# Performance work log

Measured on AMD Instinct MI355X. Metric: run time of the kernel, lower is better.

The kernel has to match this reference:

```python
import jax, jax.numpy as jnp
import numpy as np

# NCHW 3x3 conv, padding=1. BatchNorm (inference affine) is folded into conv weight/bias,
# which is mathematically identical to Conv->BN(eval) in the original.
def conv3(x, w, b, stride):
    y = jax.lax.conv_general_dilated(x, w, (stride, stride), [(1, 1), (1, 1)],
                                     dimension_numbers=('NCHW', 'OIHW', 'NCHW'))
    return y + b[None, :, None, None]

def lin1(x, w, b):  # 1x1 conv as channel matmul; w: [out, in]
    return jnp.einsum('oc,bchw->bohw', w, x) + b[None, :, None, None]

def setup_inputs():
    key = jax.random.key(0)
    ks = list(jax.random.split(key, 32))
    C, M = 32, 32  # cv_hypo_num, mid_dim (kq_dim == mid_dim since mid_dim <= 128)
    B, H, W = 1, 256, 512
    w3 = lambda k, o, i: jax.random.normal(k, (o, i, 3, 3), jnp.float32) * 0.05
    w1 = lambda k, o, i: jax.random.normal(k, (o, i), jnp.float32) * 0.05
    bv = lambda k, o: jax.random.normal(k, (o,), jnp.float32) * 0.01
    inp = {
        'mono_pseudo_cost': jax.random.normal(ks[0], (B, C, H, W), jnp.float32),
        'cost_volume': jax.random.normal(ks[1], (B, C, H, W), jnp.float32),
        # mono_expand / multi_expand: two stride-2 conv(+folded BN)+ReLU blocks each
        'me_w1': w3(ks[2], M, C), 'me_b1': bv(ks[3], M),
        'me_w2': w3(ks[4], M, C), 'me_b2': bv(ks[5], M),
        'xe_w1': w3(ks[6], M, C), 'xe_b1': bv(ks[7], M),
        'xe_w2': w3(ks[8], M, C), 'xe_b2': bv(ks[9], M),
        # 1x1 q/k/v projections for both branches
        'mq_w': w1(ks[10], M, M), 'mq_b': bv(ks[11], M),
        'mk_w': w1(ks[12], M, M), 'mk_b': bv(ks[13], M),
        'mv_w': w1(ks[14], M, M), 'mv_b': bv(ks[15], M),
        'xq_w': w1(ks[16], M, M), 'xq_b': bv(ks[17], M),
        'xk_w': w1(ks[18], M, M), 'xk_b': bv(ks[19], M),
        'xv_w': w1(ks[20], M, M), 'xv_b': bv(ks[21], M),
        # residual branches
        'mr_w1': w3(ks[22], M, C), 'mr_b1': bv(ks[23], M),
        'mr_w2': w3(ks[24], M, C), 'mr_b2': bv(ks[25], M),
        'xr_w': w1(ks[26], M, C), 'xr_b': bv(ks[27], M),
        'gamma': jnp.full((1,), 0.5, jnp.float32),  # nonzero so attention path is live
    }
    return inp

def reference(mono_pseudo_cost, cost_volume,
              me_w1, me_b1, me_w2, me_b2,
              xe_w1, xe_b1, xe_w2, xe_b2,
              mq_w, mq_b, mk_w, mk_b, mv_w, mv_b,
              xq_w, xq_b, xk_w, xk_b, xv_w, xv_b,
              mr_w1, mr_b1, mr_w2, mr_b2,
              xr_w, xr_b, gamma):
    relu = jax.nn.relu
    init_h, init_w = cost_volume.shape[2], cost_volume.shape[3]
    M = me_w1.shape[0]
    # feature extractors (stride-2 x2): [B,32,256,512] -> [B,32,64,128]
    mono_feat = relu(conv3(relu(conv3(mono_pseudo_cost, me_w1, me_b1, 2)), me_w2, me_b2, 2))
    multi_feat = relu(conv3(relu(conv3(cost_volume, xe_w1, xe_b1, 2)), xe_w2, xe_b2, 2))
    b, c, h, w = multi_feat.shape
    hw = h * w
    # q/k/v as [B, C, hw]
    mono_q = lin1(mono_feat, mq_w, mq_b).reshape(b, -1, hw)
    mono_k = lin1(mono_feat, mk_w, mk_b).reshape(b, -1, hw)
    mono_v = lin1(mono_feat, mv_w, mv_b).reshape(b, -1, hw)
    multi_q = lin1(multi_feat, xq_w, xq_b).reshape(b, -1, hw)
    multi_k = lin1(multi_feat, xk_w, xk_b).reshape(b, -1, hw)
    multi_v = lin1(multi_feat, xv_w, xv_b).reshape(b, -1, hw)
    # full [B, hw, hw] attention, no 1/sqrt(d) scaling (as in original)
    mono_atten = jax.nn.softmax(jnp.einsum('bci,bcj->bij', mono_q, mono_k), axis=-1)
    multi_atten = jax.nn.softmax(jnp.einsum('bci,bcj->bij', multi_q, multi_k), axis=-1)
    # cross application: mono values weighted by multi attention and vice versa
    mono_out = jnp.einsum('bcj,bij->bci', mono_v, multi_atten).reshape(b, M, h, w)
    multi_out = jnp.einsum('bcj,bij->bci', multi_v, mono_atten).reshape(b, M, h, w)
    fused = jnp.concatenate([multi_out, mono_out], axis=1)
    # nearest-neighbor upsample back to input size (integer factor 4)
    fused = jnp.repeat(jnp.repeat(fused, init_h // h, axis=2), init_w // w, axis=3)
    # residual branches
    mono_residual = relu(conv3(relu(conv3(mono_pseudo_cost, mr_w1, mr_b1, 1)), mr_w2, mr_b2, 1))
    multi_residual = relu(lin1(cost_volume, xr_w, xr_b))
    fused = jnp.concatenate([mono_residual, multi_residual], axis=1) + gamma * fused
    return fused
```

## Files before the change

### kernel.cpp

```cpp
#include <hip/hip_runtime.h>


using bf16x8 = __attribute__((ext_vector_type(8))) short;
using f32x4  = __attribute__((ext_vector_type(4))) float;
using f32x16 = __attribute__((ext_vector_type(16))) float;
typedef unsigned short u16;
typedef unsigned int   u32;

__device__ __forceinline__ u16 f2bf(float f) {
  u32 u = __builtin_bit_cast(u32, f);
  u = (u + 0x7fffu + ((u >> 16) & 1u)) >> 16;
  return (u16)u;
}
__device__ __forceinline__ float bf2f(u16 v) {
  u32 u = ((u32)v) << 16;
  return __builtin_bit_cast(float, u);
}
__device__ __forceinline__ u32 pktr(float lo, float hi) {
  return __builtin_amdgcn_perm(__builtin_bit_cast(u32, hi),
                               __builtin_bit_cast(u32, lo), 0x07060302u);
}
__device__ __forceinline__ f32x4 mfma16(bf16x8 a, bf16x8 b, f32x4 c) {
  return __builtin_amdgcn_mfma_f32_16x16x32_bf16(a, b, c, 0, 0, 0);
}
__device__ __forceinline__ f32x16 mfma32(bf16x8 a, bf16x8 b, f32x16 c) {
  return __builtin_amdgcn_mfma_f32_32x32x16_bf16(a, b, c, 0, 0, 0);
}
__device__ __forceinline__ f32x16 zero16() {
  f32x16 z = {0,0,0,0,0,0,0,0,0,0,0,0,0,0,0,0};
  return z;
}
__device__ __forceinline__ void store4bf(u16* dst, f32x4 v) {
  u32 lo = (u32)f2bf(v[0]) | ((u32)f2bf(v[1]) << 16);
  u32 hi = (u32)f2bf(v[2]) | ((u32)f2bf(v[3]) << 16);
  *(uint2*)dst = make_uint2(lo, hi);
}

struct WPtrs { const float* p[13]; };

__global__ void k_pre(WPtrs wp, u16* __restrict__ wConv, u16* __restrict__ w1x1,
                      const float* __restrict__ mono, const float* __restrict__ cv,
                      u16* __restrict__ monoT, u16* __restrict__ cvT,
                      u16* __restrict__ m1T, u16* __restrict__ x1T, u16* __restrict__ r1T) {
  int bx = blockIdx.x, t = threadIdx.x;
  if (bx < 13) {
    if (bx < 6) {
      const float* s = wp.p[bx];
      u16* d = wConv + bx * 9216;
      for (int i = t; i < 9216; i += 256) {
        int tap = i >> 10, co = (i >> 5) & 31, ci = i & 31;
        d[i] = f2bf(s[co * 288 + ci * 9 + tap]);
      }
    } else {
      const float* s = wp.p[bx];
      u16* d = w1x1 + (bx - 6) * 1024;
      for (int i = t; i < 1024; i += 256) d[i] = f2bf(s[i]);
    }
    return;
  }
  if (bx < 138) {
    int zb = bx - 13;
    int buf = zb % 5, blk = zb / 5;
    u16* b; int Hp, Wp;
    switch (buf) {
      case 0: b = monoT; Hp = 258; Wp = 514; break;
      case 1: b = cvT;   Hp = 258; Wp = 514; break;
      case 2: b = m1T;   Hp = 130; Wp = 258; break;
      case 3: b = x1T;   Hp = 130; Wp = 258; break;
      default: b = r1T;  Hp = 258; Wp = 514; break;
    }
    int id = blk * 256 + t;
    int cell = id >> 2, c8 = (id & 3) << 3;
    if (cell >= 2 * (Hp + Wp)) return;
    int r, c;
    if (cell < Wp)              { r = 0;                 c = cell; }
    else if (cell < 2 * Wp)     { r = Hp - 1;            c = cell - Wp; }
    else if (cell < 2 * Wp + Hp){ r = cell - 2 * Wp;     c = 0; }
    else                        { r = cell - 2 * Wp - Hp; c = Wp - 1; }
    bf16x8 z = {0, 0, 0, 0, 0, 0, 0, 0};
    *(bf16x8*)&b[(r * Wp + c) * 32 + c8] = z;
    return;
  }
  int idx = bx - 138;
  int xb = idx & 7, y = (idx >> 3) & 255, z = idx >> 11;
  const float* src = z ? cv : mono;
  u16* dst = z ? cvT : monoT;
  int x0 = xb << 6;
  __shared__ u16 tile[64][40];
  int ci = t >> 3, kx = (t & 7) << 3;
  const float* sp = src + ci * 131072 + y * 512 + x0 + kx;
  float4 a = *(const float4*)sp;
  float4 bb = *(const float4*)(sp + 4);
  tile[kx + 0][ci] = f2bf(a.x); tile[kx + 1][ci] = f2bf(a.y);
  tile[kx + 2][ci] = f2bf(a.z); tile[kx + 3][ci] = f2bf(a.w);
  tile[kx + 4][ci] = f2bf(bb.x); tile[kx + 5][ci] = f2bf(bb.y);
  tile[kx + 6][ci] = f2bf(bb.z); tile[kx + 7][ci] = f2bf(bb.w);
  __syncthreads();
  int x = t >> 2, c8 = (t & 3) << 3;
  bf16x8 v = *(bf16x8*)&tile[x][c8];
  *(bf16x8*)(dst + ((y + 1) * 514 + (x0 + x + 1)) * 32 + c8) = v;
}

__device__ __forceinline__ void conv3x3_body(int bxl, int tid,
    const u16* __restrict__ inT, int Wp, const u16* __restrict__ w9,
    const float* __restrict__ bias, u16* __restrict__ out, int outPitch,
    int outOff, int Ho, int tprShift, int stride) {
  int wid = (bxl * 256 + tid) >> 6;
  int lane = tid & 63, ln = lane & 15, q = lane >> 4;
  int y = wid >> tprShift;
  int x0 = (wid & ((1 << tprShift) - 1)) << 4;
  if (y >= Ho) return;
  f32x4 acc0 = *(const f32x4*)(bias + q * 4);
  f32x4 acc1 = *(const f32x4*)(bias + 16 + q * 4);
  const u16* ib = inT + (stride * y * Wp + stride * (x0 + ln)) * 32 + q * 8;
  const u16* wb = w9 + ln * 32 + q * 8;
#pragma unroll
  for (int dy = 0; dy < 3; ++dy)
#pragma unroll
    for (int dx = 0; dx < 3; ++dx) {
      int tap = dy * 3 + dx;
      bf16x8 bf = *(const bf16x8*)(ib + (dy * Wp + dx) * 32);
      acc0 = mfma16(*(const bf16x8*)(wb + tap * 1024), bf, acc0);
      acc1 = mfma16(*(const bf16x8*)(wb + tap * 1024 + 512), bf, acc1);
    }
#pragma unroll
  for (int r = 0; r < 4; ++r) { acc0[r] = fmaxf(acc0[r], 0.f); acc1[r] = fmaxf(acc1[r], 0.f); }
  u16* ob = out + (outOff + y * outPitch + x0 + ln) * 32;
  store4bf(ob + q * 4, acc0);
  store4bf(ob + 16 + q * 4, acc1);
}

__global__ void k_convs(const u16* __restrict__ monoT, const u16* __restrict__ cvT,
                        const u16* __restrict__ wConv,
                        const float* me_b1, const float* xe_b1, const float* mr_b1,
                        u16* __restrict__ m1T, u16* __restrict__ x1T, u16* __restrict__ r1T) {
  int bx = blockIdx.x;
  if (bx < 512)
    conv3x3_body(bx, threadIdx.x, monoT, 514, wConv + 0 * 9216, me_b1, m1T, 258, 259, 128, 4, 2);
  else if (bx < 1024)
    conv3x3_body(bx - 512, threadIdx.x, cvT, 514, wConv + 2 * 9216, xe_b1, x1T, 258, 259, 128, 4, 2);
  else
    conv3x3_body(bx - 1024, threadIdx.x, monoT, 514, wConv + 4 * 9216, mr_b1, r1T, 514, 515, 256, 5, 1);
}

__global__ void k_feat(const u16* __restrict__ m1T, const u16* __restrict__ x1T,
                       const u16* __restrict__ wConv,
                       const float* me_b2, const float* xe_b2,
                       u16* __restrict__ featM, u16* __restrict__ featX) {
  int bx = blockIdx.x;
  if (bx < 128)
    conv3x3_body(bx, threadIdx.x, m1T, 258, wConv + 1 * 9216, me_b2, featM, 128, 0, 64, 3, 2);
  else
    conv3x3_body(bx - 128, threadIdx.x, x1T, 258, wConv + 3 * 9216, xe_b2, featX, 128, 0, 64, 3, 2);
}

__global__ void k_proj(const u16* __restrict__ featM, const u16* __restrict__ featX,
                       const u16* __restrict__ w1x1,
                       const float* mq_b, const float* mk_b, const float* mv_b,
                       const float* xq_b, const float* xk_b, const float* xv_b,
                       u16* Qm, u16* Km, u16* Vm, u16* Qx, u16* Kx, u16* Vx) {
  int which = blockIdx.y;
  const u16* feat = (which < 3) ? featM : featX;
  const float* bias; u16* dst; float scale = 1.f; int cmode = 0;
  switch (which) {
    case 0: bias = mq_b; dst = Qm; scale = 1.4426950408889634f; break;
    case 1: bias = mk_b; dst = Km; break;
    case 2: bias = mv_b; dst = Vm; cmode = 1; break;
    case 3: bias = xq_b; dst = Qx; scale = 1.4426950408889634f; break;
    case 4: bias = xk_b; dst = Kx; break;
    default: bias = xv_b; dst = Vx; cmode = 1; break;
  }
  const u16* w = w1x1 + which * 1024;
  int wave = threadIdx.x >> 6, lane = threadIdx.x & 63, ln = lane & 15, q = lane >> 4;
  int p0 = (blockIdx.x * 4 + wave) << 4;
  bf16x8 bf = *(const bf16x8*)(feat + (p0 + ln) * 32 + q * 8);
  bf16x8 a0 = *(const bf16x8*)(w + ln * 32 + q * 8);
  bf16x8 a1 = *(const bf16x8*)(w + (16 + ln) * 32 + q * 8);
  f32x4 acc0 = *(const f32x4*)(bias + q * 4);
  f32x4 acc1 = *(const f32x4*)(bias + 16 + q * 4);
  acc0 = mfma16(a0, bf, acc0);
  acc1 = mfma16(a1, bf, acc1);
#pragma unroll
  for (int r = 0; r < 4; ++r) { acc0[r] *= scale; acc1[r] *= scale; }
  if (!cmode) {
    store4bf(dst + (p0 + ln) * 32 + q * 4, acc0);
    store4bf(dst + (p0 + ln) * 32 + 16 + q * 4, acc1);
  } else {
    int p = p0 + ln;
    int jl = p & 63, jb = p & ~63;
    int pj = jb + (jl >> 5) * 32 + ((jl >> 4) & 1) * 16 + ((jl >> 2) & 1) * 8
           + ((jl >> 3) & 1) * 4 + (jl & 3);
#pragma unroll
    for (int r = 0; r < 4; ++r) {
      dst[(q * 4 + r) * 8192 + pj] = f2bf(acc0[r]);
      dst[(16 + q * 4 + r) * 8192 + pj] = f2bf(acc1[r]);
    }
  }
}

__global__ void __launch_bounds__(256, 4) k_attention(
    const u16* __restrict__ Qm, const u16* __restrict__ Km, const u16* __restrict__ Vm,
    const u16* __restrict__ Qx, const u16* __restrict__ Kx, const u16* __restrict__ Vx,
    u16* __restrict__ Opart, float* __restrict__ lpart) {
  const u16 *Qp, *Kp, *Vp;
  int att = blockIdx.z;
  if (att == 0) { Qp = Qm; Kp = Km; Vp = Vx; }
  else          { Qp = Qx; Kp = Kx; Vp = Vm; }
  int sp = blockIdx.y;
  int j0 = sp << 10;

  __shared__ u16 Kl[2][64][40];
  __shared__ u16 Vl[2][32][72];

  int t = threadIdx.x, wave = t >> 6, lane = t & 63, ln = lane & 31, h = lane >> 5;
  int iw = blockIdx.x * 128 + wave * 32;

  bf16x8 qf0 = *(const bf16x8*)(Qp + (iw + ln) * 32 + h * 8);
  bf16x8 qf1 = *(const bf16x8*)(Qp + (iw + ln) * 32 + 16 + h * 8);

  int krow = t >> 2, kcol = (t & 3) << 3;
  int vrow = t >> 3, vcol = (t & 7) << 3;
  const u16* Kg = Kp + j0 * 32;
  const u16* Vg = Vp + j0;

  bf16x8 kn = *(const bf16x8*)(Kg + t * 8);
  bf16x8 vn = *(const bf16x8*)(Vg + vrow * 8192 + vcol);
  *(bf16x8*)&Kl[0][krow][kcol] = kn;
  *(bf16x8*)&Vl[0][vrow][vcol] = vn;

  f32x16 O = zero16(), lac = zero16();
  const short oneb = 0x3F80;
  const bf16x8 ones = {oneb, oneb, oneb, oneb, oneb, oneb, oneb, oneb};

  for (int jt = 0; jt < 16; ++jt) {
    __syncthreads();
    bool have = (jt + 1) < 16;
    if (have) {
      kn = *(const bf16x8*)(Kg + (jt + 1) * 2048 + t * 8);
      vn = *(const bf16x8*)(Vg + vrow * 8192 + (jt + 1) * 64 + vcol);
    }
    int cur = jt & 1;
    f32x16 s0 = mfma32(*(const bf16x8*)&Kl[cur][ln][h * 8], qf0, zero16());
    s0 = mfma32(*(const bf16x8*)&Kl[cur][ln][16 + h * 8], qf1, s0);
    f32x16 s1 = mfma32(*(const bf16x8*)&Kl[cur][32 + ln][h * 8], qf0, zero16());
    s1 = mfma32(*(const bf16x8*)&Kl[cur][32 + ln][16 + h * 8], qf1, s1);
    float e0[16], e1[16];
#pragma unroll
    for (int r = 0; r < 16; ++r) {
      e0[r] = __builtin_amdgcn_exp2f(s0[r]);
      e1[r] = __builtin_amdgcn_exp2f(s1[r]);
    }
    union PF { bf16x8 v; u32 w[4]; } pf[4];
#pragma unroll
    for (int t2 = 0; t2 < 4; ++t2) {
      int base = (t2 & 1) * 8;
      if (t2 < 2) {
#pragma unroll
        for (int p = 0; p < 4; ++p) pf[t2].w[p] = pktr(e0[base + 2 * p], e0[base + 2 * p + 1]);
      } else {
#pragma unroll
        for (int p = 0; p < 4; ++p) pf[t2].w[p] = pktr(e1[base + 2 * p], e1[base + 2 * p + 1]);
      }
    }
#pragma unroll
    for (int t2 = 0; t2 < 4; ++t2) {
      bf16x8 vf = *(const bf16x8*)&Vl[cur][ln][t2 * 16 + h * 8];
      O = mfma32(pf[t2].v, vf, O);
      lac = mfma32(pf[t2].v, ones, lac);
    }
    if (have) {
      *(bf16x8*)&Kl[1 - cur][krow][kcol] = kn;
      *(bf16x8*)&Vl[1 - cur][vrow][vcol] = vn;
    }
  }
  u16* ob = Opart + (size_t)(att * 8 + sp) * 262144;
  float* lb = lpart + (att * 8 + sp) * 8192;
#pragma unroll
  for (int r = 0; r < 16; ++r) {
    int ig = iw + (r & 3) + 8 * (r >> 2) + 4 * h;
    ob[ig * 32 + ln] = f2bf(O[r]);
    if (ln == 0) lb[ig] = lac[r];
  }
}

__global__ void k_reduce(const u16* __restrict__ Opart, const float* __restrict__ lpart,
                         float* __restrict__ attA, float* __restrict__ attB) {
  int a = blockIdx.y;
  int id = blockIdx.x * 256 + threadIdx.x;
  int i = id >> 5, c = id & 31;
  float s = 0.f, l = 0.f;
#pragma unroll
  for (int sp = 0; sp < 8; ++sp) {
    s += bf2f(Opart[(size_t)(a * 8 + sp) * 262144 + id]);
    l += lpart[(a * 8 + sp) * 8192 + i];
  }
  float* out = a ? attB : attA;
  out[i * 32 + c] = s / l;
}

__global__ void k_final(const u16* __restrict__ r1T, const u16* __restrict__ cvT,
                        const u16* __restrict__ wConv, const u16* __restrict__ w1x1,
                        const float* mr_b2, const float* xr_b,
                        const float* __restrict__ attA, const float* __restrict__ attB,
                        const float* __restrict__ gamma, float* __restrict__ dout) {
  int bx = blockIdx.x, tid = threadIdx.x;
  int lane = tid & 63, ln = lane & 15, q = lane >> 4;
  float g = gamma[0];
  if (bx < 2048) {
    const u16* w9 = wConv + 5 * 9216;
    int wid = (bx * 256 + tid) >> 6;
    int y = wid >> 5, x0 = (wid & 31) << 4;
    f32x4 acc0 = *(const f32x4*)(mr_b2 + q * 4);
    f32x4 acc1 = *(const f32x4*)(mr_b2 + 16 + q * 4);
    const u16* ib = r1T + (y * 514 + x0 + ln) * 32 + q * 8;
    const u16* wb = w9 + ln * 32 + q * 8;
#pragma unroll
    for (int dy = 0; dy < 3; ++dy)
#pragma unroll
      for (int dx = 0; dx < 3; ++dx) {
        int tap = dy * 3 + dx;
        bf16x8 bf = *(const bf16x8*)(ib + (dy * 514 + dx) * 32);
        acc0 = mfma16(*(const bf16x8*)(wb + tap * 1024), bf, acc0);
        acc1 = mfma16(*(const bf16x8*)(wb + tap * 1024 + 512), bf, acc1);
      }
    int xg = x0 + ln;
    const float* ap = attA + ((y >> 2) * 128 + (xg >> 2)) * 32;
    float* ob = dout + y * 512 + xg;
#pragma unroll
    for (int r = 0; r < 4; ++r) {
      int co0 = q * 4 + r, co1 = 16 + q * 4 + r;
      ob[co0 * 131072] = fmaxf(acc0[r], 0.f) + g * ap[co0];
      ob[co1 * 131072] = fmaxf(acc1[r], 0.f) + g * ap[co1];
    }
  } else {
    const u16* w = w1x1 + 6 * 1024;
    int wid = ((bx - 2048) * 256 + tid) >> 6;
    int p0 = wid << 4;
    int y = p0 >> 9, x0 = p0 & 511;
    bf16x8 bf = *(const bf16x8*)(cvT + ((y + 1) * 514 + x0 + ln + 1) * 32 + q * 8);
    f32x4 acc0 = *(const f32x4*)(xr_b + q * 4);
    f32x4 acc1 = *(const f32x4*)(xr_b + 16 + q * 4);
    acc0 = mfma16(*(const bf16x8*)(w + ln * 32 + q * 8), bf, acc0);
    acc1 = mfma16(*(const bf16x8*)(w + (16 + ln) * 32 + q * 8), bf, acc1);
    int xg = x0 + ln;
    const float* ap = attB + ((y >> 2) * 128 + (xg >> 2)) * 32;
    float* ob = dout + 32 * 131072 + p0 + ln;
#pragma unroll
    for (int r = 0; r < 4; ++r) {
      int co0 = q * 4 + r, co1 = 16 + q * 4 + r;
      ob[co0 * 131072] = fmaxf(acc0[r], 0.f) + g * ap[co0];
      ob[co1 * 131072] = fmaxf(acc1[r], 0.f) + g * ap[co1];
    }
  }
}

extern "C" void kernel_launch(void* const* d_in, const int* in_sizes, int n_in,
                              void* d_out, int out_size, void* d_ws, size_t ws_size,
                              hipStream_t stream) {
  const float* mono  = (const float*)d_in[0];
  const float* cv    = (const float*)d_in[1];
  const float* me_b1 = (const float*)d_in[3];
  const float* me_b2 = (const float*)d_in[5];
  const float* xe_b1 = (const float*)d_in[7];
  const float* xe_b2 = (const float*)d_in[9];
  const float* mq_b  = (const float*)d_in[11];
  const float* mk_b  = (const float*)d_in[13];
  const float* mv_b  = (const float*)d_in[15];
  const float* xq_b  = (const float*)d_in[17];
  const float* xk_b  = (const float*)d_in[19];
  const float* xv_b  = (const float*)d_in[21];
  const float* mr_b2 = (const float*)d_in[25];
  const float* mr_b1 = (const float*)d_in[23];
  const float* xr_b  = (const float*)d_in[27];
  const float* gamma = (const float*)d_in[28];
  float* dout = (float*)d_out;

  char* ws = (char*)d_ws;
  u16* wConv = (u16*)(ws + 0);
  u16* w1x1  = (u16*)(ws + 110592);
  u16* monoT = (u16*)(ws + 124928);
  u16* Opart = (u16*)(ws + 124928);
  u16* cvT   = (u16*)(ws + 8612096);
  u16* m1T   = (u16*)(ws + 17099264);
  u16* x1T   = (u16*)(ws + 19245824);
  u16* r1T   = (u16*)(ws + 21392384);
  u16* featM = (u16*)(ws + 29879552);
  u16* featX = (u16*)(ws + 30403840);
  u16* Qm    = (u16*)(ws + 30928128);
  u16* Km    = (u16*)(ws + 31452416);
  u16* Vm    = (u16*)(ws + 31976704);
  u16* Qx    = (u16*)(ws + 32500992);
  u16* Kx    = (u16*)(ws + 33025280);
  u16* Vx    = (u16*)(ws + 33549568);
  float* attA  = (float*)(ws + 34073856);
  float* attB  = (float*)(ws + 35122432);
  float* lpart = (float*)(ws + 36171008);

  WPtrs wp;
  wp.p[0] = (const float*)d_in[2];
  wp.p[1] = (const float*)d_in[4];
  wp.p[2] = (const float*)d_in[6];
  wp.p[3] = (const float*)d_in[8];
  wp.p[4] = (const float*)d_in[22];
  wp.p[5] = (const float*)d_in[24];
  wp.p[6] = (const float*)d_in[10];
  wp.p[7] = (const float*)d_in[12];
  wp.p[8] = (const float*)d_in[14];
  wp.p[9] = (const float*)d_in[16];
  wp.p[10] = (const float*)d_in[18];
  wp.p[11] = (const float*)d_in[20];
  wp.p[12] = (const float*)d_in[26];

  k_pre<<<4234, 256, 0, stream>>>(wp, wConv, w1x1, mono, cv, monoT, cvT, m1T, x1T, r1T);
  k_convs<<<3072, 256, 0, stream>>>(monoT, cvT, wConv, me_b1, xe_b1, mr_b1, m1T, x1T, r1T);
  k_feat<<<256, 256, 0, stream>>>(m1T, x1T, wConv, me_b2, xe_b2, featM, featX);
  k_proj<<<dim3(128, 6), 256, 0, stream>>>(featM, featX, w1x1,
                                           mq_b, mk_b, mv_b, xq_b, xk_b, xv_b,
                                           Qm, Km, Vm, Qx, Kx, Vx);
  k_attention<<<dim3(64, 8, 2), 256, 0, stream>>>(Qm, Km, Vm, Qx, Kx, Vx, Opart, lpart);
  k_reduce<<<dim3(1024, 2), 256, 0, stream>>>(Opart, lpart, attA, attB);
  k_final<<<4096, 256, 0, stream>>>(r1T, cvT, wConv, w1x1, mr_b2, xr_b, attA, attB, gamma, dout);
}
```

Before: 213.2 us.

## Merge pipeline into cooperative persistent megakernel with grid syncs and fused stages

Replaces the seven-kernel chain with one cooperative persistent kernel that walks the stages with grid-stride virtual blocks and grid.sync between them, and falls back to five stage kernels if the cooperative launch fails. It also fuses the second stride-2 conv with the q/k/v projections through LDS, which drops the feat buffers, and fuses the partial-attention reduction into the final output stage through an LDS tile, which drops the attA/attB buffers. The aim is to cut launch gaps and intermediate global traffic. In exchange it adds grid-wide barrier cost, caps occupancy at 4 blocks per CU, and makes every stage share one LDS union.

Measured after the change: 543.5 us. 155% more time.

```diff
diff --git a/kernel.cpp b/kernel.cpp
--- a/kernel.cpp
+++ b/kernel.cpp
@@ -1,4 +1,7 @@
 #include <hip/hip_runtime.h>
+#include <hip/hip_cooperative_groups.h>
+
+namespace cg = cooperative_groups;
 
 
 using bf16x8 = __attribute__((ext_vector_type(8))) short;
@@ -36,70 +39,24 @@
   *(uint2*)dst = make_uint2(lo, hi);
 }
 
-struct WPtrs { const float* p[13]; };
-
-__global__ void k_pre(WPtrs wp, u16* __restrict__ wConv, u16* __restrict__ w1x1,
-                      const float* __restrict__ mono, const float* __restrict__ cv,
-                      u16* __restrict__ monoT, u16* __restrict__ cvT,
-                      u16* __restrict__ m1T, u16* __restrict__ x1T, u16* __restrict__ r1T) {
-  int bx = blockIdx.x, t = threadIdx.x;
-  if (bx < 13) {
-    if (bx < 6) {
-      const float* s = wp.p[bx];
-      u16* d = wConv + bx * 9216;
-      for (int i = t; i < 9216; i += 256) {
-        int tap = i >> 10, co = (i >> 5) & 31, ci = i & 31;
-        d[i] = f2bf(s[co * 288 + ci * 9 + tap]);
-      }
-    } else {
-      const float* s = wp.p[bx];
-      u16* d = w1x1 + (bx - 6) * 1024;
-      for (int i = t; i < 1024; i += 256) d[i] = f2bf(s[i]);
-    }
-    return;
-  }
-  if (bx < 138) {
-    int zb = bx - 13;
-    int buf = zb % 5, blk = zb / 5;
-    u16* b; int Hp, Wp;
-    switch (buf) {
-      case 0: b = monoT; Hp = 258; Wp = 514; break;
-      case 1: b = cvT;   Hp = 258; Wp = 514; break;
-      case 2: b = m1T;   Hp = 130; Wp = 258; break;
-      case 3: b = x1T;   Hp = 130; Wp = 258; break;
-      default: b = r1T;  Hp = 258; Wp = 514; break;
-    }
-    int id = blk * 256 + t;
-    int cell = id >> 2, c8 = (id & 3) << 3;
-    if (cell >= 2 * (Hp + Wp)) return;
-    int r, c;
-    if (cell < Wp)              { r = 0;                 c = cell; }
-    else if (cell < 2 * Wp)     { r = Hp - 1;            c = cell - Wp; }
-    else if (cell < 2 * Wp + Hp){ r = cell - 2 * Wp;     c = 0; }
-    else                        { r = cell - 2 * Wp - Hp; c = Wp - 1; }
-    bf16x8 z = {0, 0, 0, 0, 0, 0, 0, 0};
-    *(bf16x8*)&b[(r * Wp + c) * 32 + c8] = z;
-    return;
-  }
-  int idx = bx - 138;
-  int xb = idx & 7, y = (idx >> 3) & 255, z = idx >> 11;
-  const float* src = z ? cv : mono;
-  u16* dst = z ? cvT : monoT;
-  int x0 = xb << 6;
-  __shared__ u16 tile[64][40];
-  int ci = t >> 3, kx = (t & 7) << 3;
-  const float* sp = src + ci * 131072 + y * 512 + x0 + kx;
-  float4 a = *(const float4*)sp;
-  float4 bb = *(const float4*)(sp + 4);
-  tile[kx + 0][ci] = f2bf(a.x); tile[kx + 1][ci] = f2bf(a.y);
-  tile[kx + 2][ci] = f2bf(a.z); tile[kx + 3][ci] = f2bf(a.w);
-  tile[kx + 4][ci] = f2bf(bb.x); tile[kx + 5][ci] = f2bf(bb.y);
-  tile[kx + 6][ci] = f2bf(bb.z); tile[kx + 7][ci] = f2bf(bb.w);
-  __syncthreads();
-  int x = t >> 2, c8 = (t & 3) << 3;
-  bf16x8 v = *(bf16x8*)&tile[x][c8];
-  *(bf16x8*)(dst + ((y + 1) * 514 + (x0 + x + 1)) * 32 + c8) = v;
-}
+struct MegaArgs {
+  const float* mono; const float* cv;
+  const float* wsrc[13];
+  const float *me_b1, *xe_b1, *mr_b1, *me_b2, *xe_b2;
+  const float *mq_b, *mk_b, *mv_b, *xq_b, *xk_b, *xv_b;
+  const float *mr_b2, *xr_b, *gamma;
+  u16 *wConv, *w1x1, *monoT, *cvT, *m1T, *x1T, *r1T;
+  u16 *Qm, *Km, *Vm, *Qx, *Kx, *Vx, *Opart;
+  float* lpart;
+  float* dout;
+};
+
+union SLDS {
+  u16 tr[64][40];
+  struct { u16 Kl[2][64][40]; u16 Vl[2][32][72]; } att;
+  u16 fp[4][16][40];
+  float fin[16][32];
+};
 
 __device__ __forceinline__ void conv3x3_body(int bxl, int tid,
     const u16* __restrict__ inT, int Wp, const u16* __restrict__ w9,
@@ -130,294 +87,383 @@
   store4bf(ob + 16 + q * 4, acc1);
 }
 
-__global__ void k_convs(const u16* __restrict__ monoT, const u16* __restrict__ cvT,
-                        const u16* __restrict__ wConv,
-                        const float* me_b1, const float* xe_b1, const float* mr_b1,
-                        u16* __restrict__ m1T, u16* __restrict__ x1T, u16* __restrict__ r1T) {
-  int bx = blockIdx.x;
-  if (bx < 512)
-    conv3x3_body(bx, threadIdx.x, monoT, 514, wConv + 0 * 9216, me_b1, m1T, 258, 259, 128, 4, 2);
-  else if (bx < 1024)
-    conv3x3_body(bx - 512, threadIdx.x, cvT, 514, wConv + 2 * 9216, xe_b1, x1T, 258, 259, 128, 4, 2);
-  else
-    conv3x3_body(bx - 1024, threadIdx.x, monoT, 514, wConv + 4 * 9216, mr_b1, r1T, 514, 515, 256, 5, 1);
-}
-
-__global__ void k_feat(const u16* __restrict__ m1T, const u16* __restrict__ x1T,
-                       const u16* __restrict__ wConv,
-                       const float* me_b2, const float* xe_b2,
-                       u16* __restrict__ featM, u16* __restrict__ featX) {
-  int bx = blockIdx.x;
-  if (bx < 128)
-    conv3x3_body(bx, threadIdx.x, m1T, 258, wConv + 1 * 9216, me_b2, featM, 128, 0, 64, 3, 2);
-  else
-    conv3x3_body(bx - 128, threadIdx.x, x1T, 258, wConv + 3 * 9216, xe_b2, featX, 128, 0, 64, 3, 2);
-}
-
-__global__ void k_proj(const u16* __restrict__ featM, const u16* __restrict__ featX,
-                       const u16* __restrict__ w1x1,
-                       const float* mq_b, const float* mk_b, const float* mv_b,
-                       const float* xq_b, const float* xk_b, const float* xv_b,
-                       u16* Qm, u16* Km, u16* Vm, u16* Qx, u16* Kx, u16* Vx) {
-  int which = blockIdx.y;
-  const u16* feat = (which < 3) ? featM : featX;
-  const float* bias; u16* dst; float scale = 1.f; int cmode = 0;
-  switch (which) {
-    case 0: bias = mq_b; dst = Qm; scale = 1.4426950408889634f; break;
-    case 1: bias = mk_b; dst = Km; break;
-    case 2: bias = mv_b; dst = Vm; cmode = 1; break;
-    case 3: bias = xq_b; dst = Qx; scale = 1.4426950408889634f; break;
-    case 4: bias = xk_b; dst = Kx; break;
-    default: bias = xv_b; dst = Vx; cmode = 1; break;
-  }
-  const u16* w = w1x1 + which * 1024;
-  int wave = threadIdx.x >> 6, lane = threadIdx.x & 63, ln = lane & 15, q = lane >> 4;
-  int p0 = (blockIdx.x * 4 + wave) << 4;
-  bf16x8 bf = *(const bf16x8*)(feat + (p0 + ln) * 32 + q * 8);
-  bf16x8 a0 = *(const bf16x8*)(w + ln * 32 + q * 8);
-  bf16x8 a1 = *(const bf16x8*)(w + (16 + ln) * 32 + q * 8);
-  f32x4 acc0 = *(const f32x4*)(bias + q * 4);
-  f32x4 acc1 = *(const f32x4*)(bias + 16 + q * 4);
-  acc0 = mfma16(a0, bf, acc0);
-  acc1 = mfma16(a1, bf, acc1);
-#pragma unroll
-  for (int r = 0; r < 4; ++r) { acc0[r] *= scale; acc1[r] *= scale; }
-  if (!cmode) {
-    store4bf(dst + (p0 + ln) * 32 + q * 4, acc0);
-    store4bf(dst + (p0 + ln) * 32 + 16 + q * 4, acc1);
-  } else {
-    int p = p0 + ln;
-    int jl = p & 63, jb = p & ~63;
-    int pj = jb + (jl >> 5) * 32 + ((jl >> 4) & 1) * 16 + ((jl >> 2) & 1) * 8
-           + ((jl >> 3) & 1) * 4 + (jl & 3);
-#pragma unroll
-    for (int r = 0; r < 4; ++r) {
-      dst[(q * 4 + r) * 8192 + pj] = f2bf(acc0[r]);
-      dst[(16 + q * 4 + r) * 8192 + pj] = f2bf(acc1[r]);
-    }
-  }
-}
-
-__global__ void __launch_bounds__(256, 4) k_attention(
-    const u16* __restrict__ Qm, const u16* __restrict__ Km, const u16* __restrict__ Vm,
-    const u16* __restrict__ Qx, const u16* __restrict__ Kx, const u16* __restrict__ Vx,
-    u16* __restrict__ Opart, float* __restrict__ lpart) {
-  const u16 *Qp, *Kp, *Vp;
-  int att = blockIdx.z;
-  if (att == 0) { Qp = Qm; Kp = Km; Vp = Vx; }
-  else          { Qp = Qx; Kp = Kx; Vp = Vm; }
-  int sp = blockIdx.y;
-  int j0 = sp << 10;
-
-  __shared__ u16 Kl[2][64][40];
-  __shared__ u16 Vl[2][32][72];
-
-  int t = threadIdx.x, wave = t >> 6, lane = t & 63, ln = lane & 31, h = lane >> 5;
-  int iw = blockIdx.x * 128 + wave * 32;
-
-  bf16x8 qf0 = *(const bf16x8*)(Qp + (iw + ln) * 32 + h * 8);
-  bf16x8 qf1 = *(const bf16x8*)(Qp + (iw + ln) * 32 + 16 + h * 8);
-
-  int krow = t >> 2, kcol = (t & 3) << 3;
-  int vrow = t >> 3, vcol = (t & 7) << 3;
-  const u16* Kg = Kp + j0 * 32;
-  const u16* Vg = Vp + j0;
-
-  bf16x8 kn = *(const bf16x8*)(Kg + t * 8);
-  bf16x8 vn = *(const bf16x8*)(Vg + vrow * 8192 + vcol);
-  *(bf16x8*)&Kl[0][krow][kcol] = kn;
-  *(bf16x8*)&Vl[0][vrow][vcol] = vn;
-
-  f32x16 O = zero16(), lac = zero16();
-  const short oneb = 0x3F80;
-  const bf16x8 ones = {oneb, oneb, oneb, oneb, oneb, oneb, oneb, oneb};
-
-  for (int jt = 0; jt < 16; ++jt) {
-    __syncthreads();
-    bool have = (jt + 1) < 16;
-    if (have) {
-      kn = *(const bf16x8*)(Kg + (jt + 1) * 2048 + t * 8);
-      vn = *(const bf16x8*)(Vg + vrow * 8192 + (jt + 1) * 64 + vcol);
-    }
-    int cur = jt & 1;
-    f32x16 s0 = mfma32(*(const bf16x8*)&Kl[cur][ln][h * 8], qf0, zero16());
-    s0 = mfma32(*(const bf16x8*)&Kl[cur][ln][16 + h * 8], qf1, s0);
-    f32x16 s1 = mfma32(*(const bf16x8*)&Kl[cur][32 + ln][h * 8], qf0, zero16());
-    s1 = mfma32(*(const bf16x8*)&Kl[cur][32 + ln][16 + h * 8], qf1, s1);
-    float e0[16], e1[16];
-#pragma unroll
-    for (int r = 0; r < 16; ++r) {
-      e0[r] = __builtin_amdgcn_exp2f(s0[r]);
-      e1[r] = __builtin_amdgcn_exp2f(s1[r]);
-    }
-    union PF { bf16x8 v; u32 w[4]; } pf[4];
-#pragma unroll
-    for (int t2 = 0; t2 < 4; ++t2) {
-      int base = (t2 & 1) * 8;
-      if (t2 < 2) {
-#pragma unroll
-        for (int p = 0; p < 4; ++p) pf[t2].w[p] = pktr(e0[base + 2 * p], e0[base + 2 * p + 1]);
+__device__ void stage0(const MegaArgs& a, SLDS& lds) {
+  int t = threadIdx.x;
+  for (int vb = blockIdx.x; vb < 4234; vb += gridDim.x) {
+    if (vb < 13) {
+      if (vb < 6) {
+        const float* s = a.wsrc[vb];
+        u16* d = a.wConv + vb * 9216;
+        for (int i = t; i < 9216; i += 256) {
+          int tap = i >> 10, co = (i >> 5) & 31, ci = i & 31;
+          d[i] = f2bf(s[co * 288 + ci * 9 + tap]);
+        }
       } else {
-#pragma unroll
-        for (int p = 0; p < 4; ++p) pf[t2].w[p] = pktr(e1[base + 2 * p], e1[base + 2 * p + 1]);
-      }
-    }
-#pragma unroll
-    for (int t2 = 0; t2 < 4; ++t2) {
-      bf16x8 vf = *(const bf16x8*)&Vl[cur][ln][t2 * 16 + h * 8];
-      O = mfma32(pf[t2].v, vf, O);
-      lac = mfma32(pf[t2].v, ones, lac);
-    }
-    if (have) {
-      *(bf16x8*)&Kl[1 - cur][krow][kcol] = kn;
-      *(bf16x8*)&Vl[1 - cur][vrow][vcol] = vn;
-    }
-  }
-  u16* ob = Opart + (size_t)(att * 8 + sp) * 262144;
-  float* lb = lpart + (att * 8 + sp) * 8192;
-#pragma unroll
-  for (int r = 0; r < 16; ++r) {
-    int ig = iw + (r & 3) + 8 * (r >> 2) + 4 * h;
-    ob[ig * 32 + ln] = f2bf(O[r]);
-    if (ln == 0) lb[ig] = lac[r];
-  }
-}
-
-__global__ void k_reduce(const u16* __restrict__ Opart, const float* __restrict__ lpart,
-                         float* __restrict__ attA, float* __restrict__ attB) {
-  int a = blockIdx.y;
-  int id = blockIdx.x * 256 + threadIdx.x;
-  int i = id >> 5, c = id & 31;
-  float s = 0.f, l = 0.f;
-#pragma unroll
-  for (int sp = 0; sp < 8; ++sp) {
-    s += bf2f(Opart[(size_t)(a * 8 + sp) * 262144 + id]);
-    l += lpart[(a * 8 + sp) * 8192 + i];
-  }
-  float* out = a ? attB : attA;
-  out[i * 32 + c] = s / l;
-}
-
-__global__ void k_final(const u16* __restrict__ r1T, const u16* __restrict__ cvT,
-                        const u16* __restrict__ wConv, const u16* __restrict__ w1x1,
-                        const float* mr_b2, const float* xr_b,
-                        const float* __restrict__ attA, const float* __restrict__ attB,
-                        const float* __restrict__ gamma, float* __restrict__ dout) {
-  int bx = blockIdx.x, tid = threadIdx.x;
-  int lane = tid & 63, ln = lane & 15, q = lane >> 4;
-  float g = gamma[0];
-  if (bx < 2048) {
-    const u16* w9 = wConv + 5 * 9216;
-    int wid = (bx * 256 + tid) >> 6;
-    int y = wid >> 5, x0 = (wid & 31) << 4;
-    f32x4 acc0 = *(const f32x4*)(mr_b2 + q * 4);
-    f32x4 acc1 = *(const f32x4*)(mr_b2 + 16 + q * 4);
-    const u16* ib = r1T + (y * 514 + x0 + ln) * 32 + q * 8;
+        const float* s = a.wsrc[vb];
+        u16* d = a.w1x1 + (vb - 6) * 1024;
+        for (int i = t; i < 1024; i += 256) d[i] = f2bf(s[i]);
+      }
+    } else if (vb < 138) {
+      int zb = vb - 13;
+      int buf = zb % 5, blk = zb / 5;
+      u16* b; int Hp, Wp;
+      switch (buf) {
+        case 0: b = a.monoT; Hp = 258; Wp = 514; break;
+        case 1: b = a.cvT;   Hp = 258; Wp = 514; break;
+        case 2: b = a.m1T;   Hp = 130; Wp = 258; break;
+        case 3: b = a.x1T;   Hp = 130; Wp = 258; break;
+        default: b = a.r1T;  Hp = 258; Wp = 514; break;
+      }
+      int id = blk * 256 + t;
+      int cell = id >> 2, c8 = (id & 3) << 3;
+      if (cell < 2 * (Hp + Wp)) {
+        int r, c;
+        if (cell < Wp)               { r = 0;                  c = cell; }
+        else if (cell < 2 * Wp)      { r = Hp - 1;             c = cell - Wp; }
+        else if (cell < 2 * Wp + Hp) { r = cell - 2 * Wp;      c = 0; }
+        else                         { r = cell - 2 * Wp - Hp; c = Wp - 1; }
+        bf16x8 z = {0, 0, 0, 0, 0, 0, 0, 0};
+        *(bf16x8*)&b[(r * Wp + c) * 32 + c8] = z;
+      }
+    } else {
+      int idx = vb - 138;
+      int xb = idx & 7, y = (idx >> 3) & 255, z = idx >> 11;
+      const float* src = z ? a.cv : a.mono;
+      u16* dst = z ? a.cvT : a.monoT;
+      int x0 = xb << 6;
+      int ci = t >> 3, kx = (t & 7) << 3;
+      const float* sp = src + ci * 131072 + y * 512 + x0 + kx;
+      float4 p = *(const float4*)sp;
+      float4 p2 = *(const float4*)(sp + 4);
+      lds.tr[kx + 0][ci] = f2bf(p.x);  lds.tr[kx + 1][ci] = f2bf(p.y);
+      lds.tr[kx + 2][ci] = f2bf(p.z);  lds.tr[kx + 3][ci] = f2bf(p.w);
+      lds.tr[kx + 4][ci] = f2bf(p2.x); lds.tr[kx + 5][ci] = f2bf(p2.y);
+      lds.tr[kx + 6][ci] = f2bf(p2.z); lds.tr[kx + 7][ci] = f2bf(p2.w);
+      __syncthreads();
+      int x = t >> 2, c8 = (t & 3) << 3;
+      bf16x8 v = *(bf16x8*)&lds.tr[x][c8];
+      *(bf16x8*)(dst + ((y + 1) * 514 + (x0 + x + 1)) * 32 + c8) = v;
+      __syncthreads();
+    }
+  }
+}
+
+__device__ void stage1(const MegaArgs& a) {
+  int t = threadIdx.x;
+  for (int vb = blockIdx.x; vb < 3072; vb += gridDim.x) {
+    if (vb < 512)
+      conv3x3_body(vb, t, a.monoT, 514, a.wConv + 0 * 9216, a.me_b1, a.m1T, 258, 259, 128, 4, 2);
+    else if (vb < 1024)
+      conv3x3_body(vb - 512, t, a.cvT, 514, a.wConv + 2 * 9216, a.xe_b1, a.x1T, 258, 259, 128, 4, 2);
+    else
+      conv3x3_body(vb - 1024, t, a.monoT, 514, a.wConv + 4 * 9216, a.mr_b1, a.r1T, 514, 515, 256, 5, 1);
+  }
+}
+
+__device__ void stage2(const MegaArgs& a, SLDS& lds) {
+  int t = threadIdx.x;
+  for (int vb = blockIdx.x; vb < 256; vb += gridDim.x) {
+    int branch = vb >> 7;
+    int bxl = vb & 127;
+    const u16* inT = branch ? a.x1T : a.m1T;
+    const u16* w9 = a.wConv + (branch ? 3 : 1) * 9216;
+    const float* cb = branch ? a.xe_b2 : a.me_b2;
+    int wave = t >> 6, lane = t & 63, ln = lane & 15, q = lane >> 4;
+    int wid = bxl * 4 + wave;
+    int y = wid >> 3, x0 = (wid & 7) << 4;
+    f32x4 acc0 = *(const f32x4*)(cb + q * 4);
+    f32x4 acc1 = *(const f32x4*)(cb + 16 + q * 4);
+    const u16* ib = inT + (2 * y * 258 + 2 * (x0 + ln)) * 32 + q * 8;
     const u16* wb = w9 + ln * 32 + q * 8;
 #pragma unroll
     for (int dy = 0; dy < 3; ++dy)
 #pragma unroll
       for (int dx = 0; dx < 3; ++dx) {
         int tap = dy * 3 + dx;
-        bf16x8 bf = *(const bf16x8*)(ib + (dy * 514 + dx) * 32);
+        bf16x8 bf = *(const bf16x8*)(ib + (dy * 258 + dx) * 32);
         acc0 = mfma16(*(const bf16x8*)(wb + tap * 1024), bf, acc0);
         acc1 = mfma16(*(const bf16x8*)(wb + tap * 1024 + 512), bf, acc1);
       }
-    int xg = x0 + ln;
-    const float* ap = attA + ((y >> 2) * 128 + (xg >> 2)) * 32;
-    float* ob = dout + y * 512 + xg;
-#pragma unroll
-    for (int r = 0; r < 4; ++r) {
-      int co0 = q * 4 + r, co1 = 16 + q * 4 + r;
-      ob[co0 * 131072] = fmaxf(acc0[r], 0.f) + g * ap[co0];
-      ob[co1 * 131072] = fmaxf(acc1[r], 0.f) + g * ap[co1];
-    }
-  } else {
-    const u16* w = w1x1 + 6 * 1024;
-    int wid = ((bx - 2048) * 256 + tid) >> 6;
-    int p0 = wid << 4;
-    int y = p0 >> 9, x0 = p0 & 511;
-    bf16x8 bf = *(const bf16x8*)(cvT + ((y + 1) * 514 + x0 + ln + 1) * 32 + q * 8);
-    f32x4 acc0 = *(const f32x4*)(xr_b + q * 4);
-    f32x4 acc1 = *(const f32x4*)(xr_b + 16 + q * 4);
-    acc0 = mfma16(*(const bf16x8*)(w + ln * 32 + q * 8), bf, acc0);
-    acc1 = mfma16(*(const bf16x8*)(w + (16 + ln) * 32 + q * 8), bf, acc1);
-    int xg = x0 + ln;
-    const float* ap = attB + ((y >> 2) * 128 + (xg >> 2)) * 32;
-    float* ob = dout + 32 * 131072 + p0 + ln;
-#pragma unroll
-    for (int r = 0; r < 4; ++r) {
-      int co0 = q * 4 + r, co1 = 16 + q * 4 + r;
-      ob[co0 * 131072] = fmaxf(acc0[r], 0.f) + g * ap[co0];
-      ob[co1 * 131072] = fmaxf(acc1[r], 0.f) + g * ap[co1];
-    }
-  }
-}
+#pragma unroll
+    for (int r = 0; r < 4; ++r) { acc0[r] = fmaxf(acc0[r], 0.f); acc1[r] = fmaxf(acc1[r], 0.f); }
+    u16* fpw = &lds.fp[wave][0][0];
+    store4bf(fpw + ln * 40 + q * 4, acc0);
+    store4bf(fpw + ln * 40 + 16 + q * 4, acc1);
+    bf16x8 bfrag = *(const bf16x8*)(fpw + ln * 40 + q * 8);
+    int p0 = wid * 16;
+    const float* qb = branch ? a.xq_b : a.mq_b;
+    const float* kb = branch ? a.xk_b : a.mk_b;
+    const float* vbias = branch ? a.xv_b : a.mv_b;
+    u16* Qd = branch ? a.Qx : a.Qm;
+    u16* Kd = branch ? a.Kx : a.Km;
+    u16* Vd = branch ? a.Vx : a.Vm;
+    int wbase = branch * 3;
+#pragma unroll
+    for (int pj3 = 0; pj3 < 3; ++pj3) {
+      const u16* w = a.w1x1 + (wbase + pj3) * 1024;
+      const float* bias = pj3 == 0 ? qb : (pj3 == 1 ? kb : vbias);
+      bf16x8 wa0 = *(const bf16x8*)(w + ln * 32 + q * 8);
+      bf16x8 wa1 = *(const bf16x8*)(w + (16 + ln) * 32 + q * 8);
+      f32x4 c0 = *(const f32x4*)(bias + q * 4);
+      f32x4 c1 = *(const f32x4*)(bias + 16 + q * 4);
+      c0 = mfma16(wa0, bfrag, c0);
+      c1 = mfma16(wa1, bfrag, c1);
+      if (pj3 == 0) {
+#pragma unroll
+        for (int r = 0; r < 4; ++r) { c0[r] *= 1.4426950408889634f; c1[r] *= 1.4426950408889634f; }
+      }
+      if (pj3 < 2) {
+        u16* dst = pj3 == 0 ? Qd : Kd;
+        store4bf(dst + (p0 + ln) * 32 + q * 4, c0);
+        store4bf(dst + (p0 + ln) * 32 + 16 + q * 4, c1);
+      } else {
+        int p = p0 + ln;
+        int jl = p & 63, jb = p & ~63;
+        int pj = jb + (jl >> 5) * 32 + ((jl >> 4) & 1) * 16 + ((jl >> 2) & 1) * 8
+               + ((jl >> 3) & 1) * 4 + (jl & 3);
+#pragma unroll
+        for (int r = 0; r < 4; ++r) {
+          Vd[(q * 4 + r) * 8192 + pj] = f2bf(c0[r]);
+          Vd[(16 + q * 4 + r) * 8192 + pj] = f2bf(c1[r]);
+        }
+      }
+    }
+  }
+}
+
+__device__ void stage3(const MegaArgs& a, SLDS& lds) {
+  int t = threadIdx.x;
+  for (int vb = blockIdx.x; vb < 1024; vb += gridDim.x) {
+    int ib64 = vb & 63, sp = (vb >> 6) & 7, att = vb >> 9;
+    const u16 *Qp, *Kp, *Vp;
+    if (att == 0) { Qp = a.Qm; Kp = a.Km; Vp = a.Vx; }
+    else          { Qp = a.Qx; Kp = a.Kx; Vp = a.Vm; }
+    int j0 = sp << 10;
+    int wave = t >> 6, lane = t & 63, ln = lane & 31, h = lane >> 5;
+    int iw = ib64 * 128 + wave * 32;
+    bf16x8 qf0 = *(const bf16x8*)(Qp + (iw + ln) * 32 + h * 8);
+    bf16x8 qf1 = *(const bf16x8*)(Qp + (iw + ln) * 32 + 16 + h * 8);
+    int krow = t >> 2, kcol = (t & 3) << 3;
+    int vrow = t >> 3, vcol = (t & 7) << 3;
+    const u16* Kg = Kp + j0 * 32;
+    const u16* Vg = Vp + j0;
+    bf16x8 kn = *(const bf16x8*)(Kg + t * 8);
+    bf16x8 vn = *(const bf16x8*)(Vg + vrow * 8192 + vcol);
+    *(bf16x8*)&lds.att.Kl[0][krow][kcol] = kn;
+    *(bf16x8*)&lds.att.Vl[0][vrow][vcol] = vn;
+    f32x16 O = zero16(), lac = zero16();
+    const short oneb = 0x3F80;
+    const bf16x8 ones = {oneb, oneb, oneb, oneb, oneb, oneb, oneb, oneb};
+    for (int jt = 0; jt < 16; ++jt) {
+      __syncthreads();
+      bool have = (jt + 1) < 16;
+      if (have) {
+        kn = *(const bf16x8*)(Kg + (jt + 1) * 2048 + t * 8);
+        vn = *(const bf16x8*)(Vg + vrow * 8192 + (jt + 1) * 64 + vcol);
+      }
+      int cur = jt & 1;
+      f32x16 s0 = mfma32(*(const bf16x8*)&lds.att.Kl[cur][ln][h * 8], qf0, zero16());
+      s0 = mfma32(*(const bf16x8*)&lds.att.Kl[cur][ln][16 + h * 8], qf1, s0);
+      f32x16 s1 = mfma32(*(const bf16x8*)&lds.att.Kl[cur][32 + ln][h * 8], qf0, zero16());
+      s1 = mfma32(*(const bf16x8*)&lds.att.Kl[cur][32 + ln][16 + h * 8], qf1, s1);
+      float e0[16], e1[16];
+#pragma unroll
+      for (int r = 0; r < 16; ++r) {
+        e0[r] = __builtin_amdgcn_exp2f(s0[r]);
+        e1[r] = __builtin_amdgcn_exp2f(s1[r]);
+      }
+      union PF { bf16x8 v; u32 w[4]; } pf[4];
+#pragma unroll
+      for (int t2 = 0; t2 < 4; ++t2) {
+        int base = (t2 & 1) * 8;
+        if (t2 < 2) {
+#pragma unroll
+          for (int p = 0; p < 4; ++p) pf[t2].w[p] = pktr(e0[base + 2 * p], e0[base + 2 * p + 1]);
+        } else {
+#pragma unroll
+          for (int p = 0; p < 4; ++p) pf[t2].w[p] = pktr(e1[base + 2 * p], e1[base + 2 * p + 1]);
+        }
+      }
+#pragma unroll
+      for (int t2 = 0; t2 < 4; ++t2) {
+        bf16x8 vf = *(const bf16x8*)&lds.att.Vl[cur][ln][t2 * 16 + h * 8];
+        O = mfma32(pf[t2].v, vf, O);
+        lac = mfma32(pf[t2].v, ones, lac);
+      }
+      if (have) {
+        *(bf16x8*)&lds.att.Kl[1 - cur][krow][kcol] = kn;
+        *(bf16x8*)&lds.att.Vl[1 - cur][vrow][vcol] = vn;
+      }
+    }
+    u16* ob = a.Opart + (size_t)(att * 8 + sp) * 262144;
+    float* lb = a.lpart + (att * 8 + sp) * 8192;
+#pragma unroll
+    for (int r = 0; r < 16; ++r) {
+      int ig = iw + (r & 3) + 8 * (r >> 2) + 4 * h;
+      ob[ig * 32 + ln] = f2bf(O[r]);
+      if (ln == 0) lb[ig] = lac[r];
+    }
+    __syncthreads();
+  }
+}
+
+__device__ void stage4(const MegaArgs& a, SLDS& lds) {
+  int t = threadIdx.x;
+  for (int u = blockIdx.x; u < 1024; u += gridDim.x) {
+    int half = u >> 9;
+    int tile = u & 511;
+    int tx = tile & 7, ty = tile >> 3;
+    int rbase = ty * 128 + tx * 16;
+    for (int e = t; e < 512; e += 256) {
+      int ir = e >> 5, ch = e & 31;
+      int gr = rbase + ir;
+      float os = 0.f, ls = 0.f;
+#pragma unroll
+      for (int sp = 0; sp < 8; ++sp) {
+        os += bf2f(a.Opart[(size_t)(half * 8 + sp) * 262144 + gr * 32 + ch]);
+        ls += a.lpart[(half * 8 + sp) * 8192 + gr];
+      }
+      lds.fin[ir][ch] = os / ls;
+    }
+    __syncthreads();
+    int wave = t >> 6, lane = t & 63, ln = lane & 15, q = lane >> 4;
+    int y = ty * 4 + wave;
+    float g = a.gamma[0];
+    if (half == 0) {
+      const u16* wb = a.wConv + 5 * 9216 + ln * 32 + q * 8;
+      f32x4 b0 = *(const f32x4*)(a.mr_b2 + q * 4);
+      f32x4 b1 = *(const f32x4*)(a.mr_b2 + 16 + q * 4);
+#pragma unroll
+      for (int xc = 0; xc < 4; ++xc) {
+        int x0 = tx * 64 + xc * 16;
+        f32x4 acc0 = b0, acc1 = b1;
+        const u16* ib = a.r1T + (y * 514 + x0 + ln) * 32 + q * 8;
+#pragma unroll
+        for (int dy = 0; dy < 3; ++dy)
+#pragma unroll
+          for (int dx = 0; dx < 3; ++dx) {
+            int tap = dy * 3 + dx;
+            bf16x8 bf = *(const bf16x8*)(ib + (dy * 514 + dx) * 32);
+            acc0 = mfma16(*(const bf16x8*)(wb + tap * 1024), bf, acc0);
+            acc1 = mfma16(*(const bf16x8*)(wb + tap * 1024 + 512), bf, acc1);
+          }
+        const float* ap = lds.fin[xc * 4 + (ln >> 2)];
+        float* ob = a.dout + y * 512 + x0 + ln;
+#pragma unroll
+        for (int r = 0; r < 4; ++r) {
+          int co0 = q * 4 + r, co1 = 16 + q * 4 + r;
+          ob[co0 * 131072] = fmaxf(acc0[r], 0.f) + g * ap[co0];
+          ob[co1 * 131072] = fmaxf(acc1[r], 0.f) + g * ap[co1];
+        }
+      }
+    } else {
+      const u16* w = a.w1x1 + 6 * 1024;
+      bf16x8 wa0 = *(const bf16x8*)(w + ln * 32 + q * 8);
+      bf16x8 wa1 = *(const bf16x8*)(w + (16 + ln) * 32 + q * 8);
+      f32x4 b0 = *(const f32x4*)(a.xr_b + q * 4);
+      f32x4 b1 = *(const f32x4*)(a.xr_b + 16 + q * 4);
+#pragma unroll
+      for (int xc = 0; xc < 4; ++xc) {
+        int x0 = tx * 64 + xc * 16;
+        bf16x8 bf = *(const bf16x8*)(a.cvT + ((y + 1) * 514 + x0 + ln + 1) * 32 + q * 8);
+        f32x4 c0 = mfma16(wa0, bf, b0);
+        f32x4 c1 = mfma16(wa1, bf, b1);
+        const float* ap = lds.fin[xc * 4 + (ln >> 2)];
+        float* ob = a.dout + 32 * 131072 + y * 512 + x0 + ln;
+#pragma unroll
+        for (int r = 0; r < 4; ++r) {
+          int co0 = q * 4 + r, co1 = 16 + q * 4 + r;
+          ob[co0 * 131072] = fmaxf(c0[r], 0.f) + g * ap[co0];
+          ob[co1 * 131072] = fmaxf(c1[r], 0.f) + g * ap[co1];
+        }
+      }
+    }
+    __syncthreads();
+  }
+}
+
+__global__ void __launch_bounds__(256, 4) k_mega(MegaArgs a) {
+  cg::grid_group grid = cg::this_grid();
+  __shared__ SLDS lds;
+  stage0(a, lds);  grid.sync();
+  stage1(a);       grid.sync();
+  stage2(a, lds);  grid.sync();
+  stage3(a, lds);  grid.sync();
+  stage4(a, lds);
+}
+
+__global__ void __launch_bounds__(256, 4) k_s0(MegaArgs a) { __shared__ SLDS lds; stage0(a, lds); }
+__global__ void __launch_bounds__(256, 4) k_s1(MegaArgs a) { stage1(a); }
+__global__ void __launch_bounds__(256, 4) k_s2(MegaArgs a) { __shared__ SLDS lds; stage2(a, lds); }
+__global__ void __launch_bounds__(256, 4) k_s3(MegaArgs a) { __shared__ SLDS lds; stage3(a, lds); }
+__global__ void __launch_bounds__(256, 4) k_s4(MegaArgs a) { __shared__ SLDS lds; stage4(a, lds); }
 
 extern "C" void kernel_launch(void* const* d_in, const int* in_sizes, int n_in,
                               void* d_out, int out_size, void* d_ws, size_t ws_size,
                               hipStream_t stream) {
-  const float* mono  = (const float*)d_in[0];
-  const float* cv    = (const float*)d_in[1];
-  const float* me_b1 = (const float*)d_in[3];
-  const float* me_b2 = (const float*)d_in[5];
-  const float* xe_b1 = (const float*)d_in[7];
-  const float* xe_b2 = (const float*)d_in[9];
-  const float* mq_b  = (const float*)d_in[11];
-  const float* mk_b  = (const float*)d_in[13];
-  const float* mv_b  = (const float*)d_in[15];
-  const float* xq_b  = (const float*)d_in[17];
-  const float* xk_b  = (const float*)d_in[19];
-  const float* xv_b  = (const float*)d_in[21];
-  const float* mr_b2 = (const float*)d_in[25];
-  const float* mr_b1 = (const float*)d_in[23];
-  const float* xr_b  = (const float*)d_in[27];
-  const float* gamma = (const float*)d_in[28];
-  float* dout = (float*)d_out;
-
   char* ws = (char*)d_ws;
-  u16* wConv = (u16*)(ws + 0);
-  u16* w1x1  = (u16*)(ws + 110592);
-  u16* monoT = (u16*)(ws + 124928);
-  u16* Opart = (u16*)(ws + 124928);
-  u16* cvT   = (u16*)(ws + 8612096);
-  u16* m1T   = (u16*)(ws + 17099264);
-  u16* x1T   = (u16*)(ws + 19245824);
-  u16* r1T   = (u16*)(ws + 21392384);
-  u16* featM = (u16*)(ws + 29879552);
-  u16* featX = (u16*)(ws + 30403840);
-  u16* Qm    = (u16*)(ws + 30928128);
-  u16* Km    = (u16*)(ws + 31452416);
-  u16* Vm    = (u16*)(ws + 31976704);
-  u16* Qx    = (u16*)(ws + 32500992);
-  u16* Kx    = (u16*)(ws + 33025280);
-  u16* Vx    = (u16*)(ws + 33549568);
-  float* attA  = (float*)(ws + 34073856);
-  float* attB  = (float*)(ws + 35122432);
-  float* lpart = (float*)(ws + 36171008);
-
-  WPtrs wp;
-  wp.p[0] = (const float*)d_in[2];
-  wp.p[1] = (const float*)d_in[4];
-  wp.p[2] = (const float*)d_in[6];
-  wp.p[3] = (const float*)d_in[8];
-  wp.p[4] = (const float*)d_in[22];
-  wp.p[5] = (const float*)d_in[24];
-  wp.p[6] = (const float*)d_in[10];
-  wp.p[7] = (const float*)d_in[12];
-  wp.p[8] = (const float*)d_in[14];
-  wp.p[9] = (const float*)d_in[16];
-  wp.p[10] = (const float*)d_in[18];
-  wp.p[11] = (const float*)d_in[20];
-  wp.p[12] = (const float*)d_in[26];
-
-  k_pre<<<4234, 256, 0, stream>>>(wp, wConv, w1x1, mono, cv, monoT, cvT, m1T, x1T, r1T);
-  k_convs<<<3072, 256, 0, stream>>>(monoT, cvT, wConv, me_b1, xe_b1, mr_b1, m1T, x1T, r1T);
-  k_feat<<<256, 256, 0, stream>>>(m1T, x1T, wConv, me_b2, xe_b2, featM, featX);
-  k_proj<<<dim3(128, 6), 256, 0, stream>>>(featM, featX, w1x1,
-                                           mq_b, mk_b, mv_b, xq_b, xk_b, xv_b,
-                                           Qm, Km, Vm, Qx, Kx, Vx);
-  k_attention<<<dim3(64, 8, 2), 256, 0, stream>>>(Qm, Km, Vm, Qx, Kx, Vx, Opart, lpart);
-  k_reduce<<<dim3(1024, 2), 256, 0, stream>>>(Opart, lpart, attA, attB);
-  k_final<<<4096, 256, 0, stream>>>(r1T, cvT, wConv, w1x1, mr_b2, xr_b, attA, attB, gamma, dout);
-}
+  MegaArgs m;
+  m.mono  = (const float*)d_in[0];
+  m.cv    = (const float*)d_in[1];
+  m.wsrc[0] = (const float*)d_in[2];
+  m.wsrc[1] = (const float*)d_in[4];
+  m.wsrc[2] = (const float*)d_in[6];
+  m.wsrc[3] = (const float*)d_in[8];
+  m.wsrc[4] = (const float*)d_in[22];
+  m.wsrc[5] = (const float*)d_in[24];
+  m.wsrc[6] = (const float*)d_in[10];
+  m.wsrc[7] = (const float*)d_in[12];
+  m.wsrc[8] = (const float*)d_in[14];
+  m.wsrc[9] = (const float*)d_in[16];
+  m.wsrc[10] = (const float*)d_in[18];
+  m.wsrc[11] = (const float*)d_in[20];
+  m.wsrc[12] = (const float*)d_in[26];
+  m.me_b1 = (const float*)d_in[3];
+  m.me_b2 = (const float*)d_in[5];
+  m.xe_b1 = (const float*)d_in[7];
+  m.xe_b2 = (const float*)d_in[9];
+  m.mq_b  = (const float*)d_in[11];
+  m.mk_b  = (const float*)d_in[13];
+  m.mv_b  = (const float*)d_in[15];
+  m.xq_b  = (const float*)d_in[17];
+  m.xk_b  = (const float*)d_in[19];
+  m.xv_b  = (const float*)d_in[21];
+  m.mr_b1 = (const float*)d_in[23];
+  m.mr_b2 = (const float*)d_in[25];
+  m.xr_b  = (const float*)d_in[27];
+  m.gamma = (const float*)d_in[28];
+  m.wConv = (u16*)(ws + 0);
+  m.w1x1  = (u16*)(ws + 110592);
+  m.monoT = (u16*)(ws + 124928);
+  m.Opart = (u16*)(ws + 124928);
+  m.cvT   = (u16*)(ws + 8612096);
+  m.m1T   = (u16*)(ws + 17099264);
+  m.x1T   = (u16*)(ws + 19245824);
+  m.r1T   = (u16*)(ws + 21392384);
+  m.Qm    = (u16*)(ws + 30928128);
+  m.Km    = (u16*)(ws + 31452416);
+  m.Vm    = (u16*)(ws + 31976704);
+  m.Qx    = (u16*)(ws + 32500992);
+  m.Kx    = (u16*)(ws + 33025280);
+  m.Vx    = (u16*)(ws + 33549568);
+  m.lpart = (float*)(ws + 36171008);
+  m.dout  = (float*)d_out;
+
+  hipError_t err = hipErrorUnknown;
+  int occ = 0;
+  if (hipOccupancyMaxActiveBlocksPerMultiprocessor(&occ, k_mega, 256, 0) == hipSuccess &&
+      occ > 0) {
+    int gridB = occ * 256;
+    if (gridB > 1024) gridB = 1024;
+    void* kargs[] = { (void*)&m };
+    err = hipLaunchCooperativeKernel((const void*)k_mega, dim3(gridB), dim3(256),
+                                     kargs, 0, stream);
+  }
+  if (err != hipSuccess) {
+    k_s0<<<4234, 256, 0, stream>>>(m);
+    k_s1<<<3072, 256, 0, stream>>>(m);
+    k_s2<<<256,  256, 0, stream>>>(m);
+    k_s3<<<1024, 256, 0, stream>>>(m);
+    k_s4<<<1024, 256, 0, stream>>>(m);
+  }
+}
```
